# Optimization experiments

Measured on AMD Instinct MI355X. Metric: run time of the kernel, lower is better.

## Reference

```python
import jax, jax.numpy as jnp
import numpy as np

EPS = 1e-5
K = 20
NH = 16
SLOPE = 0.2

def leaky(x):
    return jnp.where(x >= 0, x, SLOPE * x)

def bn(x, g, b, axes):
    # training-mode batch norm (biased variance), channel axis = 1
    m = x.mean(axes, keepdims=True)
    v = x.var(axes, keepdims=True)
    shp = [1] * x.ndim
    shp[1] = -1
    return (x - m) / jnp.sqrt(v + EPS) * g.reshape(shp) + b.reshape(shp)

def efr(x, idx, w, k):
    # x: [B, C, N]; idx: flat global gather indices [B*N*k]; w: [C_out, 2C+1]
    B, C, N = x.shape
    xt = x.transpose(0, 2, 1).reshape(B * N, C)
    feature = xt[idx].reshape(B, N, k, C)            # gathered neighbors
    xc = xt.reshape(B, N, 1, C)
    fmean = feature.mean(-1, keepdims=True)          # [B,N,k,1]
    f = jnp.concatenate([feature - xc, fmean, jnp.broadcast_to(xc, feature.shape)], axis=3)
    return jnp.einsum('bnkc,oc->bonk', f, w)         # 1x1 conv -> [B,C_out,N,k]


def setup_inputs() -> dict:
    key = jax.random.key(0)
    ks = jax.random.split(key, 24)
    B, N = 8, 4096
    IN_CH, FEAT_CH, OUT_CH = 6, 64, 64
    d = {}
    d['points'] = jax.random.normal(ks[0], (B, IN_CH // 2, N), dtype=jnp.float32)
    d['feat'] = jax.random.normal(ks[1], (B, FEAT_CH // 2, N), dtype=jnp.float32)
    d['idx'] = jax.random.randint(ks[2], (B * N * K,), 0, B * N)
    s = 0.1
    d['w_efr_p'] = jax.random.normal(ks[3], (IN_CH, IN_CH + 1), dtype=jnp.float32) * s
    d['w_efr_f'] = jax.random.normal(ks[4], (FEAT_CH, FEAT_CH + 1), dtype=jnp.float32) * s
    d['w_q'] = jax.random.normal(ks[5], (FEAT_CH, FEAT_CH // 2), dtype=jnp.float32) * s
    d['g_q'] = jnp.ones((FEAT_CH,), jnp.float32)
    d['b_q'] = jnp.zeros((FEAT_CH,), jnp.float32)
    d['w_pos1'] = jax.random.normal(ks[6], (IN_CH, IN_CH // 2), dtype=jnp.float32) * s
    d['g_pos1'] = jnp.ones((IN_CH,), jnp.float32)
    d['b_pos1'] = jnp.zeros((IN_CH,), jnp.float32)
    d['w_pos2'] = jax.random.normal(ks[7], (FEAT_CH, IN_CH), dtype=jnp.float32) * s
    d['w_attn'] = jax.random.normal(ks[8], (NH * IN_CH, FEAT_CH), dtype=jnp.float32) * s
    d['g1'] = jnp.ones((NH,), jnp.float32)
    d['b1'] = jnp.zeros((NH,), jnp.float32)
    d['w_lin'] = jax.random.normal(ks[9], (OUT_CH, NH), dtype=jnp.float32) * s
    d['g_lin'] = jnp.ones((OUT_CH,), jnp.float32)
    d['b_lin'] = jnp.zeros((OUT_CH,), jnp.float32)
    d['w_res'] = jax.random.normal(ks[10], (OUT_CH, FEAT_CH), dtype=jnp.float32) * s
    d['g_res'] = jnp.ones((OUT_CH,), jnp.float32)
    d['b_res'] = jnp.zeros((OUT_CH,), jnp.float32)
    return d


def reference(points, feat, idx, w_efr_p, w_efr_f, w_q, g_q, b_q,
              w_pos1, g_pos1, b_pos1, w_pos2, w_attn, g1, b1,
              w_lin, g_lin, b_lin, w_res, g_res, b_res):
    B, _, N = points.shape
    knn_points = efr(points, idx, w_efr_p, K)   # [B,6,N,K]
    knn_feat = efr(feat, idx, w_efr_f, K)       # [B,64,N,K]
    x_q = leaky(bn(jnp.einsum('bcn,oc->bon', feat, w_q), g_q, b_q, (0, 2)))
    pos = leaky(bn(jnp.einsum('bcn,oc->bon', points, w_pos1), g_pos1, b_pos1, (0, 2)))
    pos = pos[:, :, :, None] - knn_points       # [B,6,N,K]
    pos = jnp.einsum('bcnk,oc->bonk', pos, w_pos2)  # [B,64,N,K]
    attn = x_q[:, :, :, None] - knn_feat + pos
    attn = jax.nn.softmax(attn / float(np.sqrt(knn_feat.shape[1])), axis=-1)
    attn = jnp.einsum('bcnk,oc->bonk', attn, w_attn)  # [B,NH*6,N,K]
    attn5 = attn.transpose(0, 2, 3, 1).reshape(B, N, K, NH, -1)  # [B,N,K,NH,6]
    y = jnp.einsum('bnkhc,bcnk->bhnk', attn5, knn_points)        # [B,NH,N,K]
    y = leaky(bn(y, g1, b1, (0, 2, 3)))
    y = bn(jnp.einsum('bcnk,oc->bonk', y, w_lin), g_lin, b_lin, (0, 2, 3))
    res = bn(jnp.einsum('bcnk,oc->bonk', knn_feat, w_res), g_res, b_res, (0, 2, 3))
    y = leaky(y + res)
    return y.max(axis=-1)                        # [B,64,N]
```

## Files before the change

kernel.cpp:

```cpp
#include <hip/hip_runtime.h>

#define KNN 20
#define NN 4096
#define NPTS 32768
#define PPW 8

using short8 = __attribute__((ext_vector_type(8))) short;
using f32x4v = __attribute__((ext_vector_type(4))) float;

__device__ __forceinline__ float lrelu(float x){ return x >= 0.f ? x : 0.2f*x; }
__device__ __forceinline__ unsigned short f2b(float x){
    union { float f; unsigned u; } v; v.f = x;
    unsigned r = v.u + 0x7FFFu + ((v.u >> 16) & 1u);
    return (unsigned short)(r >> 16);
}
__device__ __forceinline__ float b2f(unsigned h){
    union { unsigned u; float f; } v; v.u = h << 16; return v.f;
}
#define WSYNC() do { asm volatile("s_waitcnt lgkmcnt(0)" ::: "memory"); __builtin_amdgcn_sched_barrier(0); } while(0)

__global__ void kprep(const float* __restrict__ weff, const float* __restrict__ wattn,
                      const float* __restrict__ wres,
                      unsigned short* __restrict__ packW, float* __restrict__ wdiff,
                      float* __restrict__ w32t)
{
    int t = threadIdx.x;
    for (int q = t; q < 1536; q += 256){
        int f = q >> 6, l = q & 63;
        const float* W; int n, rowlen, koff;
        if (f < 4){ W = weff; rowlen = 65; n = f*16 + (l&15); koff = 0; }
        else if (f < 16){ W = wattn; rowlen = 64; int ff = f-4; n = (ff>>1)*16 + (l&15); koff = (ff&1)*32; }
        else { W = wres; rowlen = 64; int ff = f-16; n = (ff>>1)*16 + (l&15); koff = (ff&1)*32; }
        #pragma unroll
        for (int j=0;j<8;j++){
            int k = koff + (j>=4?16:0) + 4*(l>>4) + (j&3);
            packW[(size_t)(f*64+l)*8 + j] = f2b(W[n*rowlen + k]);
        }
    }
    for (int q = t; q < 2048; q += 256){
        int c = q >> 5, j = q & 31;
        wdiff[q] = weff[c*65 + 33 + j] - weff[c*65 + j];
    }
    if (t < 64) w32t[t] = weff[t*65 + 32];
}

__global__ void __launch_bounds__(256) k0_prep(
    const float* __restrict__ pts, const float* __restrict__ feat,
    const float* __restrict__ wq, const float* __restrict__ wpos1,
    const float* __restrict__ wefp, const float* __restrict__ wdiff,
    unsigned short* __restrict__ ft16, float* __restrict__ pt4,
    unsigned short* __restrict__ qp16, float* __restrict__ pp,
    unsigned short* __restrict__ base16, float* __restrict__ bpp,
    float* __restrict__ qsum, float* __restrict__ qsq,
    float* __restrict__ psum, float* __restrict__ psq)
{
    __shared__ float swq[2048];
    __shared__ float swd[2048];
    __shared__ float red[4][64], red2[4][64];
    int tid = threadIdx.x;
    for (int m=tid;m<2048;m+=256){ swq[m]=wq[m]; swd[m]=wdiff[m]; }
    __syncthreads();
    int r = blockIdx.x*256 + tid;
    int b = r >> 12, n = r & 4095;
    float p0 = pts[((size_t)b*3+0)*NN+n];
    float p1 = pts[((size_t)b*3+1)*NN+n];
    float p2 = pts[((size_t)b*3+2)*NN+n];
    float pm = (p0+p1+p2)*(1.f/3.f);
    *(float4*)(pt4 + (size_t)r*4) = make_float4(p0,p1,p2,pm);
    float f[32];
    #pragma unroll
    for (int c=0;c<32;c++) f[c] = feat[((size_t)b*32+c)*NN+n];
    #pragma unroll
    for (int c=0;c<32;c+=2){
        unsigned pk = (unsigned)f2b(f[c]) | ((unsigned)f2b(f[c+1])<<16);
        *(unsigned*)(ft16 + (size_t)r*32 + c) = pk;
    }
    float q[64];
    for (int o=0;o<64;o++){
        float a=0.f;
        #pragma unroll
        for (int c=0;c<32;c++) a += swq[o*32+c]*f[c];
        q[o]=a;
    }
    for (int o=0;o<64;o+=2){
        unsigned pk = (unsigned)f2b(q[o]) | ((unsigned)f2b(q[o+1])<<16);
        *(unsigned*)(qp16 + (size_t)r*64 + o) = pk;
    }
    int lane = tid & 63, wvv = tid>>6;
    for (int o=0;o<64;o++){
        float s=q[o], s2=q[o]*q[o];
        for (int d=1; d<64; d<<=1){ s += __shfl_xor(s,d); s2 += __shfl_xor(s2,d); }
        if (lane==0){ red[wvv][o]=s; red2[wvv][o]=s2; }
    }
    __syncthreads();
    if (tid<64){
        atomicAdd(qsum+tid, red[0][tid]+red[1][tid]+red[2][tid]+red[3][tid]);
        atomicAdd(qsq+tid, red2[0][tid]+red2[1][tid]+red2[2][tid]+red2[3][tid]);
    }
    for (int o=0;o<64;o++){
        float a=0.f;
        #pragma unroll
        for (int c=0;c<32;c++) a += swd[o*32+c]*f[c];
        q[o]=a;
    }
    for (int o=0;o<64;o+=2){
        unsigned pk = (unsigned)f2b(q[o]) | ((unsigned)f2b(q[o+1])<<16);
        *(unsigned*)(base16 + (size_t)r*64 + o) = pk;
    }
    float pr[8];
    #pragma unroll
    for (int o=0;o<6;o++) pr[o] = wpos1[o*3]*p0 + wpos1[o*3+1]*p1 + wpos1[o*3+2]*p2;
    pr[6]=0.f; pr[7]=0.f;
    *(float4*)(pp+(size_t)r*8)   = make_float4(pr[0],pr[1],pr[2],pr[3]);
    *(float4*)(pp+(size_t)r*8+4) = make_float4(pr[4],pr[5],pr[6],pr[7]);
    __syncthreads();
    for (int o=0;o<6;o++){
        float s=pr[o], s2=pr[o]*pr[o];
        for (int d=1;d<64;d<<=1){ s += __shfl_xor(s,d); s2 += __shfl_xor(s2,d); }
        if (lane==0){ red[wvv][o]=s; red2[wvv][o]=s2; }
    }
    __syncthreads();
    if (tid<6){
        atomicAdd(psum+tid, red[0][tid]+red[1][tid]+red[2][tid]+red[3][tid]);
        atomicAdd(psq+tid, red2[0][tid]+red2[1][tid]+red2[2][tid]+red2[3][tid]);
    }
    #pragma unroll
    for (int j=0;j<6;j++)
        bpp[(size_t)r*8+j] = p0*(wefp[j*7+4]-wefp[j*7]) + p1*(wefp[j*7+5]-wefp[j*7+1])
                           + p2*(wefp[j*7+6]-wefp[j*7+2]);
    bpp[(size_t)r*8+6]=0.f; bpp[(size_t)r*8+7]=0.f;
}

__global__ void k1_paramsA(
    const float* __restrict__ qsum, const float* __restrict__ qsq,
    const float* __restrict__ psum, const float* __restrict__ psq,
    const float* __restrict__ gq, const float* __restrict__ bq,
    const float* __restrict__ gp, const float* __restrict__ bp,
    float* __restrict__ bnq_a, float* __restrict__ bnq_c,
    float* __restrict__ bnp_a, float* __restrict__ bnp_c)
{
    int t = threadIdx.x;
    const float inv = 1.f/32768.f;
    if (t < 64){
        float m = qsum[t]*inv; float v = qsq[t]*inv - m*m;
        float a = gq[t]*rsqrtf(v + 1e-5f);
        bnq_a[t] = a; bnq_c[t] = bq[t] - m*a;
    }
    if (t < 6){
        float m = psum[t]*inv; float v = psq[t]*inv - m*m;
        float a = gp[t]*rsqrtf(v + 1e-5f);
        bnp_a[t] = a; bnp_c[t] = bp[t] - m*a;
    }
}

#define ARENA 12032
#define ANB 0
#define ATR 2048
#define KFR 6144
#define A2B 0
#define SFM 10240
#define SSKP 10368
#define SNB4 11392
#define SIDX 11904

__global__ void __launch_bounds__(256, 3) k2_main(
    const unsigned short* __restrict__ ft16, const float* __restrict__ pt4,
    const unsigned short* __restrict__ qp16, const float* __restrict__ pp,
    const unsigned short* __restrict__ base16, const float* __restrict__ bpp,
    const int* __restrict__ idx,
    const float* __restrict__ wefp, const float* __restrict__ wpos2,
    const unsigned short* __restrict__ packW, const float* __restrict__ w32t,
    const float* __restrict__ bnq_a, const float* __restrict__ bnq_c,
    const float* __restrict__ bnp_a, const float* __restrict__ bnp_c,
    unsigned short* __restrict__ yv, unsigned short* __restrict__ rf,
    float* __restrict__ yslot, float* __restrict__ rslot)
{
    __shared__ __align__(16) char smem_[4*ARENA];
    const int tid = threadIdx.x;
    const int l = tid & 63, wv = tid >> 6;
    const int lo = l & 15, g = l >> 4;
    char* S = smem_ + wv*ARENA;

    float w2r[4][6], w32r[4];
    #pragma unroll
    for (int nt=0;nt<4;nt++){
        #pragma unroll
        for (int j=0;j<6;j++) w2r[nt][j] = wpos2[(nt*16+lo)*6+j];
        w32r[nt] = w32t[nt*16+lo];
    }
    float ysum=0.f, ysq=0.f;
    float racc[4]={0.f,0.f,0.f,0.f}, rsqa[4]={0.f,0.f,0.f,0.f};

    for (int pi=0; pi<PPW; pi++){
        const int r = blockIdx.x*(4*PPW) + wv*PPW + pi;
        WSYNC();
        if (l < KNN) *(int*)(S+SIDX+l*4) = idx[(size_t)r*KNN + l];
        WSYNC();
        #pragma unroll
        for (int it=0; it<3; it++){
            int id = it*64 + l;
            int k = id >> 3, q = id & 7;
            bool act = id < 160;
            int kk = act ? k : 0;
            int gI = *(const int*)(S+SIDX+kk*4);
            uint2 v; v.x = 0u; v.y = 0u;
            if (act) v = *(const uint2*)(ft16 + (size_t)gI*32 + q*4);
            float s = b2f(v.x & 0xffffu) + b2f(v.x >> 16) + b2f(v.y & 0xffffu) + b2f(v.y >> 16);
            s += __shfl_xor(s,1); s += __shfl_xor(s,2); s += __shfl_xor(s,4);
            if (act){
                if (q == 0) *(float*)(S+SFM+k*4) = s * (1.f/32.f);
                *(uint2*)(S + ANB + (k>>4)*1024 + ((k&15) + 16*(q&3))*16 + (q>>2)*8) = v;
            }
        }
        if (l < KNN){
            int gI = *(const int*)(S+SIDX+l*4);
            *(float4*)(S+SNB4+l*16) = *(const float4*)(pt4 + (size_t)gI*4);
        }
        WSYNC();
        if (l < KNN){
            float4 nb = *(const float4*)(S+SNB4+l*16);
            #pragma unroll
            for (int j=0;j<6;j++){
                float v = bpp[(size_t)r*8+j] + wefp[j*7]*nb.x + wefp[j*7+1]*nb.y
                        + wefp[j*7+2]*nb.z + wefp[j*7+3]*nb.w;
                *(float*)(S+SSKP + (l*8+j)*4) = v;
            }
        }
        float xqv[4], basev[4];
        #pragma unroll
        for (int nt=0;nt<4;nt++){
            int c = nt*16+lo;
            xqv[nt] = lrelu(bnq_a[c]*b2f(qp16[(size_t)r*64+c]) + bnq_c[c]);
            basev[nt] = b2f(base16[(size_t)r*64+c]);
        }
        float sp[6];
        #pragma unroll
        for (int j=0;j<6;j++) sp[j] = lrelu(bnp_a[j]*pp[(size_t)r*8+j] + bnp_c[j]);
        WSYNC();
        f32x4v C1[2][4];
        #pragma unroll
        for (int mt=0;mt<2;mt++)
            #pragma unroll
            for (int nt=0;nt<4;nt++)
                #pragma unroll
                for (int i=0;i<4;i++) C1[mt][nt][i] = 0.f;
        short8 Af[2];
        #pragma unroll
        for (int mt=0;mt<2;mt++) Af[mt] = *(const short8*)(S + ANB + mt*1024 + l*16);
        #pragma unroll
        for (int nt=0;nt<4;nt++){
            short8 Bf = *(const short8*)(packW + (size_t)(nt*64 + l)*8);
            #pragma unroll
            for (int mt=0;mt<2;mt++)
                C1[mt][nt] = __builtin_amdgcn_mfma_f32_16x16x32_bf16(Af[mt], Bf, C1[mt][nt], 0, 0, 0);
        }
        #pragma unroll
        for (int mt=0;mt<2;mt++){
            #pragma unroll
            for (int i=0;i<4;i++){
                int k = mt*16 + g*4 + i;
                bool valid = (k < KNN);
                int kk = valid ? k : 0;
                float fmk = *(const float*)(S+SFM+kk*4);
                float sk[6];
                #pragma unroll
                for (int j=0;j<6;j++) sk[j] = *(const float*)(S+SSKP+(kk*8+j)*4);
                #pragma unroll
                for (int nt=0;nt<4;nt++){
                    float kf = C1[mt][nt][i] + basev[nt] + w32r[nt]*fmk;
                    if (valid){
                        int fragi = mt*2 + (nt>>1);
                        int slot = (g*4+i) + 16*(lo>>2);
                        int jj = (nt&1)*4 + (lo&3);
                        *(unsigned short*)(S + KFR + fragi*1024 + slot*16 + jj*2) = f2b(kf);
                    }
                    float pos = 0.f;
                    #pragma unroll
                    for (int j=0;j<6;j++) pos += (sp[j]-sk[j])*w2r[nt][j];
                    C1[mt][nt][i] = valid ? (xqv[nt] - kf + pos)*0.125f : -1e30f;
                }
            }
        }
        #pragma unroll
        for (int nt=0;nt<4;nt++){
            float mx = -1e30f;
            #pragma unroll
            for (int mt=0;mt<2;mt++)
                #pragma unroll
                for (int i=0;i<4;i++) mx = fmaxf(mx, C1[mt][nt][i]);
            mx = fmaxf(mx, __shfl_xor(mx,16));
            mx = fmaxf(mx, __shfl_xor(mx,32));
            float sm = 0.f;
            #pragma unroll
            for (int mt=0;mt<2;mt++)
                #pragma unroll
                for (int i=0;i<4;i++){ float e = __expf(C1[mt][nt][i]-mx); C1[mt][nt][i]=e; sm += e; }
            sm += __shfl_xor(sm,16);
            sm += __shfl_xor(sm,32);
            float inv = 1.f/sm;
            #pragma unroll
            for (int mt=0;mt<2;mt++)
                #pragma unroll
                for (int i=0;i<4;i++){
                    int k = mt*16 + g*4 + i;
                    if (k < KNN){
                        int fragi = mt*2 + (nt>>1);
                        int slot = (g*4+i) + 16*(lo>>2);
                        int jj = (nt&1)*4 + (lo&3);
                        *(unsigned short*)(S + ATR + fragi*1024 + slot*16 + jj*2) = f2b(C1[mt][nt][i]*inv);
                    }
                }
        }
        WSYNC();
        short8 Aa[2][2];
        #pragma unroll
        for (int mt=0;mt<2;mt++)
            #pragma unroll
            for (int s=0;s<2;s++) Aa[mt][s] = *(const short8*)(S + ATR + (mt*2+s)*1024 + l*16);
        f32x4v C2[2][6];
        #pragma unroll
        for (int mt=0;mt<2;mt++)
            #pragma unroll
            for (int nt=0;nt<6;nt++)
                #pragma unroll
                for (int i=0;i<4;i++) C2[mt][nt][i] = 0.f;
        #pragma unroll
        for (int nt=0;nt<6;nt++){
            #pragma unroll
            for (int s=0;s<2;s++){
                short8 Bf = *(const short8*)(packW + (size_t)((4+nt*2+s)*64 + l)*8);
                #pragma unroll
                for (int mt=0;mt<2;mt++)
                    C2[mt][nt] = __builtin_amdgcn_mfma_f32_16x16x32_bf16(Aa[mt][s], Bf, C2[mt][nt], 0, 0, 0);
            }
        }
        WSYNC();
        #pragma unroll
        for (int mt=0;mt<2;mt++)
            #pragma unroll
            for (int nt=0;nt<6;nt++)
                #pragma unroll
                for (int i=0;i<4;i++){
                    int k = mt*16 + g*4 + i;
                    if (k < KNN){
                        int o = nt*16 + lo;
                        *(unsigned short*)(S + A2B + k*192 + o*2) = f2b(C2[mt][nt][i]);
                    }
                }
        WSYNC();
        #pragma unroll
        for (int it=0; it<5; it++){
            int kq = it*4 + g;
            const char* row = S + A2B + kq*192 + lo*12;
            unsigned d0 = *(const unsigned*)(row);
            unsigned d1 = *(const unsigned*)(row+4);
            unsigned d2 = *(const unsigned*)(row+8);
            float yval = b2f(d0&0xffffu) * (*(const float*)(S+SSKP+(kq*8+0)*4))
                       + b2f(d0>>16)    * (*(const float*)(S+SSKP+(kq*8+1)*4))
                       + b2f(d1&0xffffu)* (*(const float*)(S+SSKP+(kq*8+2)*4))
                       + b2f(d1>>16)    * (*(const float*)(S+SSKP+(kq*8+3)*4))
                       + b2f(d2&0xffffu)* (*(const float*)(S+SSKP+(kq*8+4)*4))
                       + b2f(d2>>16)    * (*(const float*)(S+SSKP+(kq*8+5)*4));
            yv[(size_t)r*320 + lo*KNN + kq] = f2b(yval);
            ysum += yval; ysq += yval*yval;
        }
        short8 Ak[2][2];
        #pragma unroll
        for (int mt=0;mt<2;mt++)
            #pragma unroll
            for (int s=0;s<2;s++) Ak[mt][s] = *(const short8*)(S + KFR + (mt*2+s)*1024 + l*16);
        f32x4v C3[2][4];
        #pragma unroll
        for (int mt=0;mt<2;mt++)
            #pragma unroll
            for (int nt=0;nt<4;nt++)
                #pragma unroll
                for (int i=0;i<4;i++) C3[mt][nt][i] = 0.f;
        #pragma unroll
        for (int nt=0;nt<4;nt++){
            #pragma unroll
            for (int s=0;s<2;s++){
                short8 Bf = *(const short8*)(packW + (size_t)((16+nt*2+s)*64 + l)*8);
                #pragma unroll
                for (int mt=0;mt<2;mt++)
                    C3[mt][nt] = __builtin_amdgcn_mfma_f32_16x16x32_bf16(Ak[mt][s], Bf, C3[mt][nt], 0, 0, 0);
            }
        }
        #pragma unroll
        for (int mt=0;mt<2;mt++)
            #pragma unroll
            for (int i=0;i<4;i++){
                int k = mt*16 + g*4 + i;
                if (k < KNN){
                    #pragma unroll
                    for (int nt=0;nt<4;nt++){
                        float v = C3[mt][nt][i];
                        rf[(size_t)r*1280 + k*64 + nt*16 + lo] = f2b(v);
                        racc[nt] += v; rsqa[nt] += v*v;
                    }
                }
            }
    }
    ysum += __shfl_xor(ysum,16); ysum += __shfl_xor(ysum,32);
    ysq  += __shfl_xor(ysq,16);  ysq  += __shfl_xor(ysq,32);
    #pragma unroll
    for (int nt=0;nt<4;nt++){
        racc[nt] += __shfl_xor(racc[nt],16); racc[nt] += __shfl_xor(racc[nt],32);
        rsqa[nt] += __shfl_xor(rsqa[nt],16); rsqa[nt] += __shfl_xor(rsqa[nt],32);
    }
    int slot = (blockIdx.x*4 + wv) & 63;
    if (l < 16){
        atomicAdd(yslot + slot*32 + l, ysum);
        #pragma unroll
        for (int nt=0;nt<4;nt++) atomicAdd(rslot + slot*128 + nt*16 + l, racc[nt]);
    } else if (l < 32){
        atomicAdd(yslot + slot*32 + 16 + lo, ysq);
        #pragma unroll
        for (int nt=0;nt<4;nt++) atomicAdd(rslot + slot*128 + 64 + nt*16 + lo, rsqa[nt]);
    }
}

__global__ void k3_paramsB(
    const float* __restrict__ yslot, const float* __restrict__ rslot,
    const float* __restrict__ g1, const float* __restrict__ b1,
    const float* __restrict__ gr, const float* __restrict__ br,
    float* __restrict__ bn1_a, float* __restrict__ bn1_c,
    float* __restrict__ bnr_a, float* __restrict__ bnr_c)
{
    __shared__ float sy[32];
    __shared__ float sr[128];
    int t = threadIdx.x;
    float s1 = 0.f;
    if (t < 32){ for (int i=0;i<64;i++) s1 += yslot[(size_t)i*32+t]; }
    float s2 = 0.f;
    for (int i=0;i<64;i++) s2 += rslot[(size_t)i*128+t];
    if (t < 32) sy[t] = s1;
    sr[t] = s2;
    __syncthreads();
    const float inv = 1.f/655360.f;
    if (t < 16){
        float m = sy[t]*inv; float v = sy[16+t]*inv - m*m;
        float a = g1[t]*rsqrtf(v + 1e-5f);
        bn1_a[t] = a; bn1_c[t] = b1[t] - m*a;
    }
    if (t < 64){
        float m = sr[t]*inv; float v = sr[64+t]*inv - m*m;
        float a = gr[t]*rsqrtf(v + 1e-5f);
        bnr_a[t] = a; bnr_c[t] = br[t] - m*a;
    }
}

__global__ void __launch_bounds__(64) k4_linstats(
    const unsigned short* __restrict__ yv,
    const float* __restrict__ bn1_a, const float* __restrict__ bn1_c,
    const float* __restrict__ wl, float* __restrict__ lslot)
{
    __shared__ float sy2[16*KNN];
    const int c = threadIdx.x;
    float wlr[16];
    #pragma unroll
    for (int h=0;h<16;h++) wlr[h] = wl[c*16+h];
    float lsum=0.f, lsq=0.f;
    for (int i=0;i<16;i++){
        size_t r = (size_t)blockIdx.x*16 + i;
        __syncthreads();
        for (int m=c; m<320; m+=64){
            float yy = b2f(yv[r*320+m]);
            int h = m/KNN;
            sy2[m] = lrelu(bn1_a[h]*yy + bn1_c[h]);
        }
        __syncthreads();
        for (int k=0;k<KNN;k++){
            float lv = 0.f;
            #pragma unroll
            for (int h=0;h<16;h++) lv += wlr[h]*sy2[h*KNN+k];
            lsum += lv; lsq += lv*lv;
        }
    }
    atomicAdd(lslot + (size_t)(blockIdx.x&255)*128 + c, lsum);
    atomicAdd(lslot + (size_t)(blockIdx.x&255)*128 + 64 + c, lsq);
}

__global__ void k5_paramsC(
    const float* __restrict__ lslot,
    const float* __restrict__ gl, const float* __restrict__ bl,
    float* __restrict__ bnl_a, float* __restrict__ bnl_c)
{
    __shared__ float sr[128];
    int t = threadIdx.x;
    float s = 0.f;
    for (int i=0;i<256;i++) s += lslot[(size_t)i*128+t];
    sr[t] = s;
    __syncthreads();
    const float inv = 1.f/655360.f;
    if (t < 64){
        float m = sr[t]*inv; float v = sr[64+t]*inv - m*m;
        float a = gl[t]*rsqrtf(v + 1e-5f);
        bnl_a[t] = a; bnl_c[t] = bl[t] - m*a;
    }
}

__global__ void __launch_bounds__(256) k6_final(
    const unsigned short* __restrict__ yv, const unsigned short* __restrict__ rf,
    const float* __restrict__ bn1_a, const float* __restrict__ bn1_c,
    const float* __restrict__ wl,
    const float* __restrict__ bnl_a, const float* __restrict__ bnl_c,
    const float* __restrict__ bnr_a, const float* __restrict__ bnr_c,
    float* __restrict__ out)
{
    __shared__ float sy2[4][16*KNN];
    __shared__ float sout[64][17];
    const int tid = threadIdx.x;
    const int w = tid >> 6, o = tid & 63;
    float wlr[16];
    #pragma unroll
    for (int h=0;h<16;h++) wlr[h] = wl[o*16+h];
    const float la = bnl_a[o], lc = bnl_c[o];
    const float ra = bnr_a[o], rc = bnr_c[o];
    const int r0 = blockIdx.x*16;
    for (int i=0;i<4;i++){
        const size_t r = (size_t)r0 + w*4 + i;
        __syncthreads();
        for (int m=o;m<320;m+=64){
            float yy = b2f(yv[r*320+m]);
            int h = m/KNN;
            sy2[w][m] = lrelu(bn1_a[h]*yy + bn1_c[h]);
        }
        __syncthreads();
        float best = -1e30f;
        for (int k=0;k<KNN;k++){
            float rv = b2f(rf[r*1280 + k*64 + o]);
            float lv = 0.f;
            #pragma unroll
            for (int h=0;h<16;h++) lv += wlr[h]*sy2[w][h*KNN+k];
            float val = lrelu(la*lv + lc + ra*rv + rc);
            best = fmaxf(best, val);
        }
        sout[o][w*4+i] = best;
    }
    __syncthreads();
    const int b = r0 >> 12, n0 = r0 & 4095;
    for (int m=tid;m<1024;m+=256){
        int oo = m >> 4, ii = m & 15;
        out[((size_t)b*64+oo)*NN + n0 + ii] = sout[oo][ii];
    }
}

extern "C" void kernel_launch(void* const* d_in, const int* in_sizes, int n_in,
                              void* d_out, int out_size, void* d_ws, size_t ws_size,
                              hipStream_t stream)
{
    const float* pts   = (const float*)d_in[0];
    const float* feat  = (const float*)d_in[1];
    const int*   idx   = (const int*)d_in[2];
    const float* wefp  = (const float*)d_in[3];
    const float* weff  = (const float*)d_in[4];
    const float* wq    = (const float*)d_in[5];
    const float* gq    = (const float*)d_in[6];
    const float* bq    = (const float*)d_in[7];
    const float* wpos1 = (const float*)d_in[8];
    const float* gp    = (const float*)d_in[9];
    const float* bp    = (const float*)d_in[10];
    const float* wpos2 = (const float*)d_in[11];
    const float* wattn = (const float*)d_in[12];
    const float* g1    = (const float*)d_in[13];
    const float* b1    = (const float*)d_in[14];
    const float* wl    = (const float*)d_in[15];
    const float* gl    = (const float*)d_in[16];
    const float* bl    = (const float*)d_in[17];
    const float* wres  = (const float*)d_in[18];
    const float* gr    = (const float*)d_in[19];
    const float* br    = (const float*)d_in[20];
    float* out = (float*)d_out;

    char* ws = (char*)d_ws;
    size_t o_ft16 = 0;
    size_t o_pt4  = o_ft16 + (size_t)NPTS*32*2;
    size_t o_qp16 = o_pt4  + (size_t)NPTS*4*4;
    size_t o_pp   = o_qp16 + (size_t)NPTS*64*2;
    size_t o_b16  = o_pp   + (size_t)NPTS*8*4;
    size_t o_bpp  = o_b16  + (size_t)NPTS*64*2;
    size_t o_packW= o_bpp  + (size_t)NPTS*8*4;
    size_t o_wdiff= o_packW + 24*512*2;
    size_t o_w32  = o_wdiff + 2048*4;
    size_t o_st   = o_w32   + 64*4;
    size_t o_qsum  = o_st;
    size_t o_qsq   = o_qsum + 64*4;
    size_t o_psum  = o_qsq  + 64*4;
    size_t o_psq   = o_psum + 8*4;
    size_t o_yslot = o_psq  + 8*4;
    size_t o_rslot = o_yslot + (size_t)64*32*4;
    size_t o_lslot = o_rslot + (size_t)64*128*4;
    size_t zero_bytes = (o_lslot + (size_t)256*128*4) - o_st;
    size_t o_par   = o_st + zero_bytes;
    size_t o_bnq_a = o_par;
    size_t o_bnq_c = o_bnq_a + 64*4;
    size_t o_bnp_a = o_bnq_c + 64*4;
    size_t o_bnp_c = o_bnp_a + 8*4;
    size_t o_bn1_a = o_bnp_c + 8*4;
    size_t o_bn1_c = o_bn1_a + 16*4;
    size_t o_bnl_a = o_bn1_c + 16*4;
    size_t o_bnl_c = o_bnl_a + 64*4;
    size_t o_bnr_a = o_bnl_c + 64*4;
    size_t o_bnr_c = o_bnr_a + 64*4;
    size_t o_yv = (o_bnr_c + 64*4 + 255) & ~(size_t)255;
    size_t o_rf = o_yv + (size_t)NPTS*320*2;

    unsigned short* ft16 = (unsigned short*)(ws + o_ft16);
    float* pt4  = (float*)(ws + o_pt4);
    unsigned short* qp16 = (unsigned short*)(ws + o_qp16);
    float* ppb  = (float*)(ws + o_pp);
    unsigned short* b16p = (unsigned short*)(ws + o_b16);
    float* bpp  = (float*)(ws + o_bpp);
    unsigned short* packW = (unsigned short*)(ws + o_packW);
    float* wdiff= (float*)(ws + o_wdiff);
    float* w32t = (float*)(ws + o_w32);
    float* qsum = (float*)(ws + o_qsum);
    float* qsq  = (float*)(ws + o_qsq);
    float* psum = (float*)(ws + o_psum);
    float* psq  = (float*)(ws + o_psq);
    float* yslot= (float*)(ws + o_yslot);
    float* rslot= (float*)(ws + o_rslot);
    float* lslot= (float*)(ws + o_lslot);
    float* bnq_a= (float*)(ws + o_bnq_a);
    float* bnq_c= (float*)(ws + o_bnq_c);
    float* bnp_a= (float*)(ws + o_bnp_a);
    float* bnp_c= (float*)(ws + o_bnp_c);
    float* bn1_a= (float*)(ws + o_bn1_a);
    float* bn1_c= (float*)(ws + o_bn1_c);
    float* bnl_a= (float*)(ws + o_bnl_a);
    float* bnl_c= (float*)(ws + o_bnl_c);
    float* bnr_a= (float*)(ws + o_bnr_a);
    float* bnr_c= (float*)(ws + o_bnr_c);
    unsigned short* yvp = (unsigned short*)(ws + o_yv);
    unsigned short* rfp = (unsigned short*)(ws + o_rf);

    hipMemsetAsync(ws + o_st, 0, zero_bytes, stream);

    kprep<<<1, 256, 0, stream>>>(weff, wattn, wres, packW, wdiff, w32t);
    k0_prep<<<128, 256, 0, stream>>>(pts, feat, wq, wpos1, wefp, wdiff,
                                     ft16, pt4, qp16, ppb, b16p, bpp,
                                     qsum, qsq, psum, psq);
    k1_paramsA<<<1, 64, 0, stream>>>(qsum, qsq, psum, psq, gq, bq, gp, bp,
                                     bnq_a, bnq_c, bnp_a, bnp_c);
    k2_main<<<NPTS/(4*PPW), 256, 0, stream>>>(ft16, pt4, qp16, ppb, b16p, bpp, idx,
                                     wefp, wpos2, packW, w32t,
                                     bnq_a, bnq_c, bnp_a, bnp_c,
                                     yvp, rfp, yslot, rslot);
    k3_paramsB<<<1, 128, 0, stream>>>(yslot, rslot, g1, b1, gr, br,
                                      bn1_a, bn1_c, bnr_a, bnr_c);
    k4_linstats<<<2048, 64, 0, stream>>>(yvp, bn1_a, bn1_c, wl, lslot);
    k5_paramsC<<<1, 128, 0, stream>>>(lslot, gl, bl, bnl_a, bnl_c);
    k6_final<<<2048, 256, 0, stream>>>(yvp, rfp, bn1_a, bn1_c, wl,
                                       bnl_a, bnl_c, bnr_a, bnr_c, out);
}
```

Baseline: 537.4 us.

## Prefetch next-point gathers, swizzle LDS fragments, stage outputs, compute linear BN stats via Gram matrix

The main kernel now preloads all gather indices once and issues the global gathers for the next point before computing the current one, so load latency overlaps with MFMA work. Fragment layouts in LDS are XOR-swizzled to reduce bank conflicts. The y and residual outputs are staged in LDS and written with vectorized nontemporal stores, and y is now stored point-major by k. Linear-layer batch-norm statistics are computed from a 16x16 Gram matrix and channel sums accumulated with MFMA, then projected through the weights in the params kernel. This adds register pressure and restructures several kernels together.

```diff
diff --git a/kernel.cpp b/kernel.cpp
--- a/kernel.cpp
+++ b/kernel.cpp
@@ -7,6 +7,7 @@
 
 using short8 = __attribute__((ext_vector_type(8))) short;
 using f32x4v = __attribute__((ext_vector_type(4))) float;
+using uint4v = __attribute__((ext_vector_type(4))) unsigned int;
 
 __device__ __forceinline__ float lrelu(float x){ return x >= 0.f ? x : 0.2f*x; }
 __device__ __forceinline__ unsigned short f2b(float x){
@@ -18,6 +19,10 @@
     union { unsigned u; float f; } v; v.u = h << 16; return v.f;
 }
 #define WSYNC() do { asm volatile("s_waitcnt lgkmcnt(0)" ::: "memory"); __builtin_amdgcn_sched_barrier(0); } while(0)
+
+__device__ __forceinline__ int fslot(int fragi, int klocal, int gp){
+    return fragi*1024 + (((klocal) + ((gp)<<4)) ^ ((gp)*5))*16;
+}
 
 __global__ void kprep(const float* __restrict__ weff, const float* __restrict__ wattn,
                       const float* __restrict__ wres,
@@ -153,15 +158,14 @@
     }
 }
 
-#define ARENA 12032
-#define ANB 0
-#define ATR 2048
-#define KFR 6144
-#define A2B 0
-#define SFM 10240
-#define SSKP 10368
-#define SNB4 11392
-#define SIDX 11904
+#define ARENA 12544
+#define ANB   0
+#define ATR   2048
+#define KFR   6272
+#define SFM   10368
+#define SSKP  10496
+#define SIDX  11136
+#define YST   11776
 
 __global__ void __launch_bounds__(256, 3) k2_main(
     const unsigned short* __restrict__ ft16, const float* __restrict__ pt4,
@@ -180,63 +184,87 @@
     const int l = tid & 63, wv = tid >> 6;
     const int lo = l & 15, g = l >> 4;
     char* S = smem_ + wv*ARENA;
-
-    float w2r[4][6], w32r[4];
+    const int srd = (l ^ (g*5))*16;
+
+    float w2r[4][6], w32r[4], bnqa[4], bnqc[4];
     #pragma unroll
     for (int nt=0;nt<4;nt++){
         #pragma unroll
         for (int j=0;j<6;j++) w2r[nt][j] = wpos2[(nt*16+lo)*6+j];
         w32r[nt] = w32t[nt*16+lo];
-    }
+        bnqa[nt] = bnq_a[nt*16+lo];
+        bnqc[nt] = bnq_c[nt*16+lo];
+    }
+    float bnpa[6], bnpc[6];
+    #pragma unroll
+    for (int j=0;j<6;j++){ bnpa[j]=bnp_a[j]; bnpc[j]=bnp_c[j]; }
+
     float ysum=0.f, ysq=0.f;
     float racc[4]={0.f,0.f,0.f,0.f}, rsqa[4]={0.f,0.f,0.f,0.f};
 
+    const int rbase = blockIdx.x*(4*PPW) + wv*PPW;
+
+    *(int*)(S+SIDX+l*4)        = idx[(size_t)rbase*KNN + l];
+    *(int*)(S+SIDX+(64+l)*4)   = idx[(size_t)rbase*KNN + 64 + l];
+    if (l < 32) *(int*)(S+SIDX+(128+l)*4) = idx[(size_t)rbase*KNN + 128 + l];
+    WSYNC();
+
+    uint2 ng0, ng1; uint2 ng2 = make_uint2(0u,0u); float4 ngp4 = make_float4(0,0,0,0);
+    unsigned short nqr[4], nbr[4];
+    float nppr[6], nbppr[6];
+    float xqv[4], basev[4], sp[6];
+
+#define ISSUE(pi_) { \
+    int sb = (pi_)*KNN*4; size_t rr = (size_t)(rbase + (pi_)); \
+    int i0 = *(const int*)(S+SIDX+sb+(l>>3)*4); \
+    int i1 = *(const int*)(S+SIDX+sb+(8+(l>>3))*4); \
+    ng0 = *(const uint2*)(ft16 + (size_t)i0*32 + (l&7)*4); \
+    ng1 = *(const uint2*)(ft16 + (size_t)i1*32 + (l&7)*4); \
+    if (l < 32){ int i2 = *(const int*)(S+SIDX+sb+(16+(l>>3))*4); \
+                 ng2 = *(const uint2*)(ft16 + (size_t)i2*32 + (l&7)*4); } \
+    if (l < KNN){ int ip = *(const int*)(S+SIDX+sb+l*4); \
+                  ngp4 = *(const float4*)(pt4 + (size_t)ip*4); } \
+    _Pragma("unroll") for (int nt=0;nt<4;nt++){ \
+        nqr[nt] = qp16[rr*64 + nt*16+lo]; nbr[nt] = base16[rr*64 + nt*16+lo]; } \
+    _Pragma("unroll") for (int j=0;j<6;j++){ nppr[j] = pp[rr*8+j]; nbppr[j] = bpp[rr*8+j]; } \
+    __builtin_amdgcn_sched_barrier(0); \
+}
+
+#define STAGE() { \
+    float s0 = b2f(ng0.x&0xffffu)+b2f(ng0.x>>16)+b2f(ng0.y&0xffffu)+b2f(ng0.y>>16); \
+    float s1 = b2f(ng1.x&0xffffu)+b2f(ng1.x>>16)+b2f(ng1.y&0xffffu)+b2f(ng1.y>>16); \
+    float s2 = b2f(ng2.x&0xffffu)+b2f(ng2.x>>16)+b2f(ng2.y&0xffffu)+b2f(ng2.y>>16); \
+    s0 += __shfl_xor(s0,1); s0 += __shfl_xor(s0,2); s0 += __shfl_xor(s0,4); \
+    s1 += __shfl_xor(s1,1); s1 += __shfl_xor(s1,2); s1 += __shfl_xor(s1,4); \
+    s2 += __shfl_xor(s2,1); s2 += __shfl_xor(s2,2); s2 += __shfl_xor(s2,4); \
+    if ((l&7)==0){ \
+        *(float*)(S+SFM+(l>>3)*4) = s0*(1.f/32.f); \
+        *(float*)(S+SFM+(8+(l>>3))*4) = s1*(1.f/32.f); \
+        if (l < 32) *(float*)(S+SFM+(16+(l>>3))*4) = s2*(1.f/32.f); \
+    } \
+    { int kk = l>>3, gp_ = l&3, jb = ((l>>2)&1)*8; \
+      *(uint2*)(S + ANB + fslot(0, kk, gp_) + jb) = ng0; \
+      *(uint2*)(S + ANB + fslot(0, 8+kk, gp_) + jb) = ng1; \
+      if (l < 32) *(uint2*)(S + ANB + fslot(1, kk, gp_) + jb) = ng2; } \
+    if (l < KNN){ \
+        _Pragma("unroll") for (int j=0;j<6;j++){ \
+            float v = nbppr[j] + wefp[j*7]*ngp4.x + wefp[j*7+1]*ngp4.y \
+                    + wefp[j*7+2]*ngp4.z + wefp[j*7+3]*ngp4.w; \
+            *(float*)(S+SSKP+(l*8+j)*4) = v; } } \
+    _Pragma("unroll") for (int nt=0;nt<4;nt++){ \
+        xqv[nt] = lrelu(bnqa[nt]*b2f(nqr[nt]) + bnqc[nt]); \
+        basev[nt] = b2f(nbr[nt]); } \
+    _Pragma("unroll") for (int j=0;j<6;j++) sp[j] = lrelu(bnpa[j]*nppr[j] + bnpc[j]); \
+    WSYNC(); \
+}
+
+    ISSUE(0);
+    STAGE();
+
     for (int pi=0; pi<PPW; pi++){
-        const int r = blockIdx.x*(4*PPW) + wv*PPW + pi;
-        WSYNC();
-        if (l < KNN) *(int*)(S+SIDX+l*4) = idx[(size_t)r*KNN + l];
-        WSYNC();
-        #pragma unroll
-        for (int it=0; it<3; it++){
-            int id = it*64 + l;
-            int k = id >> 3, q = id & 7;
-            bool act = id < 160;
-            int kk = act ? k : 0;
-            int gI = *(const int*)(S+SIDX+kk*4);
-            uint2 v; v.x = 0u; v.y = 0u;
-            if (act) v = *(const uint2*)(ft16 + (size_t)gI*32 + q*4);
-            float s = b2f(v.x & 0xffffu) + b2f(v.x >> 16) + b2f(v.y & 0xffffu) + b2f(v.y >> 16);
-            s += __shfl_xor(s,1); s += __shfl_xor(s,2); s += __shfl_xor(s,4);
-            if (act){
-                if (q == 0) *(float*)(S+SFM+k*4) = s * (1.f/32.f);
-                *(uint2*)(S + ANB + (k>>4)*1024 + ((k&15) + 16*(q&3))*16 + (q>>2)*8) = v;
-            }
-        }
-        if (l < KNN){
-            int gI = *(const int*)(S+SIDX+l*4);
-            *(float4*)(S+SNB4+l*16) = *(const float4*)(pt4 + (size_t)gI*4);
-        }
-        WSYNC();
-        if (l < KNN){
-            float4 nb = *(const float4*)(S+SNB4+l*16);
-            #pragma unroll
-            for (int j=0;j<6;j++){
-                float v = bpp[(size_t)r*8+j] + wefp[j*7]*nb.x + wefp[j*7+1]*nb.y
-                        + wefp[j*7+2]*nb.z + wefp[j*7+3]*nb.w;
-                *(float*)(S+SSKP + (l*8+j)*4) = v;
-            }
-        }
-        float xqv[4], basev[4];
-        #pragma unroll
-        for (int nt=0;nt<4;nt++){
-            int c = nt*16+lo;
-            xqv[nt] = lrelu(bnq_a[c]*b2f(qp16[(size_t)r*64+c]) + bnq_c[c]);
-            basev[nt] = b2f(base16[(size_t)r*64+c]);
-        }
-        float sp[6];
-        #pragma unroll
-        for (int j=0;j<6;j++) sp[j] = lrelu(bnp_a[j]*pp[(size_t)r*8+j] + bnp_c[j]);
-        WSYNC();
+        const size_t r = (size_t)(rbase + pi);
+        if (pi < PPW-1) ISSUE(pi+1);
+
         f32x4v C1[2][4];
         #pragma unroll
         for (int mt=0;mt<2;mt++)
@@ -244,15 +272,13 @@
             for (int nt=0;nt<4;nt++)
                 #pragma unroll
                 for (int i=0;i<4;i++) C1[mt][nt][i] = 0.f;
-        short8 Af[2];
-        #pragma unroll
-        for (int mt=0;mt<2;mt++) Af[mt] = *(const short8*)(S + ANB + mt*1024 + l*16);
+        short8 Af0 = *(const short8*)(S + ANB + 0*1024 + srd);
+        short8 Af1 = *(const short8*)(S + ANB + 1*1024 + srd);
         #pragma unroll
         for (int nt=0;nt<4;nt++){
             short8 Bf = *(const short8*)(packW + (size_t)(nt*64 + l)*8);
-            #pragma unroll
-            for (int mt=0;mt<2;mt++)
-                C1[mt][nt] = __builtin_amdgcn_mfma_f32_16x16x32_bf16(Af[mt], Bf, C1[mt][nt], 0, 0, 0);
+            C1[0][nt] = __builtin_amdgcn_mfma_f32_16x16x32_bf16(Af0, Bf, C1[0][nt], 0, 0, 0);
+            C1[1][nt] = __builtin_amdgcn_mfma_f32_16x16x32_bf16(Af1, Bf, C1[1][nt], 0, 0, 0);
         }
         #pragma unroll
         for (int mt=0;mt<2;mt++){
@@ -269,10 +295,8 @@
                 for (int nt=0;nt<4;nt++){
                     float kf = C1[mt][nt][i] + basev[nt] + w32r[nt]*fmk;
                     if (valid){
-                        int fragi = mt*2 + (nt>>1);
-                        int slot = (g*4+i) + 16*(lo>>2);
-                        int jj = (nt&1)*4 + (lo&3);
-                        *(unsigned short*)(S + KFR + fragi*1024 + slot*16 + jj*2) = f2b(kf);
+                        int fa = fslot(mt*2+(nt>>1), g*4+i, lo>>2) + ((nt&1)*4 + (lo&3))*2;
+                        *(unsigned short*)(S + KFR + fa) = f2b(kf);
                     }
                     float pos = 0.f;
                     #pragma unroll
@@ -304,10 +328,8 @@
                 for (int i=0;i<4;i++){
                     int k = mt*16 + g*4 + i;
                     if (k < KNN){
-                        int fragi = mt*2 + (nt>>1);
-                        int slot = (g*4+i) + 16*(lo>>2);
-                        int jj = (nt&1)*4 + (lo&3);
-                        *(unsigned short*)(S + ATR + fragi*1024 + slot*16 + jj*2) = f2b(C1[mt][nt][i]*inv);
+                        int fa = fslot(mt*2+(nt>>1), g*4+i, lo>>2) + ((nt&1)*4 + (lo&3))*2;
+                        *(unsigned short*)(S + ATR + fa) = f2b(C1[mt][nt][i]*inv);
                     }
                 }
         }
@@ -316,7 +338,7 @@
         #pragma unroll
         for (int mt=0;mt<2;mt++)
             #pragma unroll
-            for (int s=0;s<2;s++) Aa[mt][s] = *(const short8*)(S + ATR + (mt*2+s)*1024 + l*16);
+            for (int s=0;s<2;s++) Aa[mt][s] = *(const short8*)(S + ATR + (mt*2+s)*1024 + srd);
         f32x4v C2[2][6];
         #pragma unroll
         for (int mt=0;mt<2;mt++)
@@ -342,16 +364,14 @@
                 #pragma unroll
                 for (int i=0;i<4;i++){
                     int k = mt*16 + g*4 + i;
-                    if (k < KNN){
-                        int o = nt*16 + lo;
-                        *(unsigned short*)(S + A2B + k*192 + o*2) = f2b(C2[mt][nt][i]);
-                    }
+                    if (k < KNN)
+                        *(unsigned short*)(S + ATR + k*208 + (nt*16+lo)*2) = f2b(C2[mt][nt][i]);
                 }
         WSYNC();
         #pragma unroll
         for (int it=0; it<5; it++){
             int kq = it*4 + g;
-            const char* row = S + A2B + kq*192 + lo*12;
+            const char* row = S + ATR + kq*208 + lo*12;
             unsigned d0 = *(const unsigned*)(row);
             unsigned d1 = *(const unsigned*)(row+4);
             unsigned d2 = *(const unsigned*)(row+8);
@@ -361,14 +381,14 @@
                        + b2f(d1>>16)    * (*(const float*)(S+SSKP+(kq*8+3)*4))
                        + b2f(d2&0xffffu)* (*(const float*)(S+SSKP+(kq*8+4)*4))
                        + b2f(d2>>16)    * (*(const float*)(S+SSKP+(kq*8+5)*4));
-            yv[(size_t)r*320 + lo*KNN + kq] = f2b(yval);
+            *(unsigned short*)(S + YST + kq*32 + lo*2) = f2b(yval);
             ysum += yval; ysq += yval*yval;
         }
         short8 Ak[2][2];
         #pragma unroll
         for (int mt=0;mt<2;mt++)
             #pragma unroll
-            for (int s=0;s<2;s++) Ak[mt][s] = *(const short8*)(S + KFR + (mt*2+s)*1024 + l*16);
+            for (int s=0;s<2;s++) Ak[mt][s] = *(const short8*)(S + KFR + (mt*2+s)*1024 + srd);
         f32x4v C3[2][4];
         #pragma unroll
         for (int mt=0;mt<2;mt++)
@@ -386,6 +406,7 @@
                     C3[mt][nt] = __builtin_amdgcn_mfma_f32_16x16x32_bf16(Ak[mt][s], Bf, C3[mt][nt], 0, 0, 0);
             }
         }
+        WSYNC();
         #pragma unroll
         for (int mt=0;mt<2;mt++)
             #pragma unroll
@@ -395,11 +416,26 @@
                     #pragma unroll
                     for (int nt=0;nt<4;nt++){
                         float v = C3[mt][nt][i];
-                        rf[(size_t)r*1280 + k*64 + nt*16 + lo] = f2b(v);
+                        *(unsigned short*)(S + ATR + k*144 + (nt*16+lo)*2) = f2b(v);
                         racc[nt] += v; rsqa[nt] += v*v;
                     }
                 }
             }
+        WSYNC();
+        if (l < 40){
+            uint4v v = *(const uint4v*)(S + YST + l*16);
+            __builtin_nontemporal_store(v, (uint4v*)((char*)yv + r*640 + l*16));
+        }
+        #pragma unroll
+        for (int t=0;t<3;t++){
+            int s = t*64 + l;
+            if (s < 160){
+                int kk = s>>3, pt_ = s&7;
+                uint4v v = *(const uint4v*)(S + ATR + kk*144 + pt_*16);
+                __builtin_nontemporal_store(v, (uint4v*)((char*)rf + r*2560 + kk*128 + pt_*16));
+            }
+        }
+        if (pi < PPW-1) STAGE();
     }
     ysum += __shfl_xor(ysum,16); ysum += __shfl_xor(ysum,32);
     ysq  += __shfl_xor(ysq,16);  ysq  += __shfl_xor(ysq,32);
@@ -418,6 +454,8 @@
         #pragma unroll
         for (int nt=0;nt<4;nt++) atomicAdd(rslot + slot*128 + 64 + nt*16 + lo, rsqa[nt]);
     }
+#undef ISSUE
+#undef STAGE
 }
 
 __global__ void k3_paramsB(
@@ -450,53 +488,93 @@
     }
 }
 
-__global__ void __launch_bounds__(64) k4_linstats(
+__global__ void __launch_bounds__(256) k4_linstats(
     const unsigned short* __restrict__ yv,
     const float* __restrict__ bn1_a, const float* __restrict__ bn1_c,
-    const float* __restrict__ wl, float* __restrict__ lslot)
-{
-    __shared__ float sy2[16*KNN];
-    const int c = threadIdx.x;
-    float wlr[16];
-    #pragma unroll
-    for (int h=0;h<16;h++) wlr[h] = wl[c*16+h];
-    float lsum=0.f, lsq=0.f;
-    for (int i=0;i<16;i++){
-        size_t r = (size_t)blockIdx.x*16 + i;
-        __syncthreads();
-        for (int m=c; m<320; m+=64){
-            float yy = b2f(yv[r*320+m]);
-            int h = m/KNN;
-            sy2[m] = lrelu(bn1_a[h]*yy + bn1_c[h]);
-        }
-        __syncthreads();
-        for (int k=0;k<KNN;k++){
-            float lv = 0.f;
-            #pragma unroll
-            for (int h=0;h<16;h++) lv += wlr[h]*sy2[h*KNN+k];
-            lsum += lv; lsq += lv*lv;
-        }
-    }
-    atomicAdd(lslot + (size_t)(blockIdx.x&255)*128 + c, lsum);
-    atomicAdd(lslot + (size_t)(blockIdx.x&255)*128 + 64 + c, lsq);
+    float* __restrict__ Mslot, float* __restrict__ Sslot)
+{
+    __shared__ __align__(16) char lds[4*1024];
+    const int tid = threadIdx.x, l = tid & 63, wvv = tid >> 6;
+    const int lo = l & 15, g = l >> 4;
+    char* L = lds + wvv*1024;
+    const int h0 = (l&1)*8;
+    float a8[8], c8[8];
+    #pragma unroll
+    for (int j=0;j<8;j++){ a8[j]=bn1_a[h0+j]; c8[j]=bn1_c[h0+j]; }
+    short8 ones;
+    #pragma unroll
+    for (int j=0;j<8;j++) ones[j] = (short)0x3F80;
+    f32x4v Macc, Sacc;
+    #pragma unroll
+    for (int i=0;i<4;i++){ Macc[i]=0.f; Sacc[i]=0.f; }
+    const int waveid = blockIdx.x*4 + wvv;
+    for (int it=0; it<5; it++){
+        size_t s0 = ((size_t)waveid*5 + it)*32;
+        uint4 v = *(const uint4*)(yv + s0*16 + l*8);
+        unsigned short e0 = v.x&0xffffu, e1 = v.x>>16, e2 = v.y&0xffffu, e3 = v.y>>16;
+        unsigned short e4 = v.z&0xffffu, e5 = v.z>>16, e6 = v.w&0xffffu, e7 = v.w>>16;
+        float y0 = lrelu(a8[0]*b2f(e0)+c8[0]), y1 = lrelu(a8[1]*b2f(e1)+c8[1]);
+        float y2_ = lrelu(a8[2]*b2f(e2)+c8[2]), y3 = lrelu(a8[3]*b2f(e3)+c8[3]);
+        float y4 = lrelu(a8[4]*b2f(e4)+c8[4]), y5 = lrelu(a8[5]*b2f(e5)+c8[5]);
+        float y6 = lrelu(a8[6]*b2f(e6)+c8[6]), y7 = lrelu(a8[7]*b2f(e7)+c8[7]);
+        uint4 o;
+        o.x = (unsigned)f2b(y0) | ((unsigned)f2b(y1)<<16);
+        o.y = (unsigned)f2b(y2_)| ((unsigned)f2b(y3)<<16);
+        o.z = (unsigned)f2b(y4) | ((unsigned)f2b(y5)<<16);
+        o.w = (unsigned)f2b(y6) | ((unsigned)f2b(y7)<<16);
+        *(uint4*)(L + l*16) = o;
+        WSYNC();
+        short8 Af;
+        #pragma unroll
+        for (int j=0;j<8;j++){
+            int s = 4*g + (j&3) + ((j>=4)?16:0);
+            Af[j] = *(const short*)(L + s*32 + lo*2);
+        }
+        WSYNC();
+        Macc = __builtin_amdgcn_mfma_f32_16x16x32_bf16(Af, Af, Macc, 0, 0, 0);
+        Sacc = __builtin_amdgcn_mfma_f32_16x16x32_bf16(ones, Af, Sacc, 0, 0, 0);
+    }
+    float* Ms = Mslot + (size_t)(waveid&15)*256;
+    #pragma unroll
+    for (int i=0;i<4;i++) atomicAdd(Ms + (g*4+i)*16 + lo, Macc[i]);
+    if (l < 16) atomicAdd(Sslot + (size_t)(waveid&15)*16 + lo, Sacc[0]);
 }
 
 __global__ void k5_paramsC(
-    const float* __restrict__ lslot,
+    const float* __restrict__ Mslot, const float* __restrict__ Sslot,
+    const float* __restrict__ wl,
     const float* __restrict__ gl, const float* __restrict__ bl,
     float* __restrict__ bnl_a, float* __restrict__ bnl_c)
 {
-    __shared__ float sr[128];
+    __shared__ float Ms[256], Ss[16];
     int t = threadIdx.x;
-    float s = 0.f;
-    for (int i=0;i<256;i++) s += lslot[(size_t)i*128+t];
-    sr[t] = s;
+    float m = 0.f;
+    for (int i=0;i<16;i++) m += Mslot[(size_t)i*256+t];
+    Ms[t] = m;
+    if (t < 16){
+        float s = 0.f;
+        for (int i=0;i<16;i++) s += Sslot[(size_t)i*16+t];
+        Ss[t] = s;
+    }
     __syncthreads();
-    const float inv = 1.f/655360.f;
     if (t < 64){
-        float m = sr[t]*inv; float v = sr[64+t]*inv - m*m;
-        float a = gl[t]*rsqrtf(v + 1e-5f);
-        bnl_a[t] = a; bnl_c[t] = bl[t] - m*a;
+        float w[16];
+        #pragma unroll
+        for (int h=0;h<16;h++) w[h] = wl[t*16+h];
+        float lsum = 0.f;
+        #pragma unroll
+        for (int h=0;h<16;h++) lsum += w[h]*Ss[h];
+        float lsq = 0.f;
+        for (int h1=0;h1<16;h1++){
+            float acc = 0.f;
+            #pragma unroll
+            for (int h2=0;h2<16;h2++) acc += Ms[h1*16+h2]*w[h2];
+            lsq += w[h1]*acc;
+        }
+        const float inv = 1.f/655360.f;
+        float mean = lsum*inv; float var = lsq*inv - mean*mean;
+        float a = gl[t]*rsqrtf(var + 1e-5f);
+        bnl_a[t] = a; bnl_c[t] = bl[t] - mean*a;
     }
 }
 
@@ -523,16 +601,17 @@
         __syncthreads();
         for (int m=o;m<320;m+=64){
             float yy = b2f(yv[r*320+m]);
-            int h = m/KNN;
+            int h = m & 15;
             sy2[w][m] = lrelu(bn1_a[h]*yy + bn1_c[h]);
         }
         __syncthreads();
         float best = -1e30f;
         for (int k=0;k<KNN;k++){
-            float rv = b2f(rf[r*1280 + k*64 + o]);
+            unsigned short rv16 = __builtin_nontemporal_load(rf + r*1280 + k*64 + o);
+            float rv = b2f(rv16);
             float lv = 0.f;
             #pragma unroll
-            for (int h=0;h<16;h++) lv += wlr[h]*sy2[w][h*KNN+k];
+            for (int h=0;h<16;h++) lv += wlr[h]*sy2[w][k*16+h];
             float val = lrelu(la*lv + lc + ra*rv + rc);
             best = fmaxf(best, val);
         }
@@ -590,8 +669,9 @@
     size_t o_psq   = o_psum + 8*4;
     size_t o_yslot = o_psq  + 8*4;
     size_t o_rslot = o_yslot + (size_t)64*32*4;
-    size_t o_lslot = o_rslot + (size_t)64*128*4;
-    size_t zero_bytes = (o_lslot + (size_t)256*128*4) - o_st;
+    size_t o_mslot = o_rslot + (size_t)64*128*4;
+    size_t o_sslot = o_mslot + (size_t)16*256*4;
+    size_t zero_bytes = (o_sslot + (size_t)16*16*4) - o_st;
     size_t o_par   = o_st + zero_bytes;
     size_t o_bnq_a = o_par;
     size_t o_bnq_c = o_bnq_a + 64*4;
@@ -611,7 +691,7 @@
     unsigned short* qp16 = (unsigned short*)(ws + o_qp16);
     float* ppb  = (float*)(ws + o_pp);
     unsigned short* b16p = (unsigned short*)(ws + o_b16);
-    float* bpp  = (float*)(ws + o_bpp);
+    float* bppb = (float*)(ws + o_bpp);
     unsigned short* packW = (unsigned short*)(ws + o_packW);
     float* wdiff= (float*)(ws + o_wdiff);
     float* w32t = (float*)(ws + o_w32);
@@ -621,7 +701,8 @@
     float* psq  = (float*)(ws + o_psq);
     float* yslot= (float*)(ws + o_yslot);
     float* rslot= (float*)(ws + o_rslot);
-    float* lslot= (float*)(ws + o_lslot);
+    float* Mslot= (float*)(ws + o_mslot);
+    float* Sslot= (float*)(ws + o_sslot);
     float* bnq_a= (float*)(ws + o_bnq_a);
     float* bnq_c= (float*)(ws + o_bnq_c);
     float* bnp_a= (float*)(ws + o_bnp_a);
@@ -635,22 +716,22 @@
     unsigned short* yvp = (unsigned short*)(ws + o_yv);
     unsigned short* rfp = (unsigned short*)(ws + o_rf);
 
-    hipMemsetAsync(ws + o_st, 0, zero_bytes, stream);
+    (void)hipMemsetAsync(ws + o_st, 0, zero_bytes, stream);
 
     kprep<<<1, 256, 0, stream>>>(weff, wattn, wres, packW, wdiff, w32t);
     k0_prep<<<128, 256, 0, stream>>>(pts, feat, wq, wpos1, wefp, wdiff,
-                                     ft16, pt4, qp16, ppb, b16p, bpp,
+                                     ft16, pt4, qp16, ppb, b16p, bppb,
                                      qsum, qsq, psum, psq);
     k1_paramsA<<<1, 64, 0, stream>>>(qsum, qsq, psum, psq, gq, bq, gp, bp,
                                      bnq_a, bnq_c, bnp_a, bnp_c);
-    k2_main<<<NPTS/(4*PPW), 256, 0, stream>>>(ft16, pt4, qp16, ppb, b16p, bpp, idx,
+    k2_main<<<NPTS/(4*PPW), 256, 0, stream>>>(ft16, pt4, qp16, ppb, b16p, bppb, idx,
                                      wefp, wpos2, packW, w32t,
                                      bnq_a, bnq_c, bnp_a, bnp_c,
                                      yvp, rfp, yslot, rslot);
     k3_paramsB<<<1, 128, 0, stream>>>(yslot, rslot, g1, b1, gr, br,
                                       bn1_a, bn1_c, bnr_a, bnr_c);
-    k4_linstats<<<2048, 64, 0, stream>>>(yvp, bn1_a, bn1_c, wl, lslot);
-    k5_paramsC<<<1, 128, 0, stream>>>(lslot, gl, bl, bnl_a, bnl_c);
+    k4_linstats<<<1024, 256, 0, stream>>>(yvp, bn1_a, bn1_c, Mslot, Sslot);
+    k5_paramsC<<<1, 256, 0, stream>>>(Mslot, Sslot, wl, gl, bl, bnl_a, bnl_c);
     k6_final<<<2048, 256, 0, stream>>>(yvp, rfp, bn1_a, bn1_c, wl,
                                        bnl_a, bnl_c, bnr_a, bnr_c, out);
 }
```

New measurement: 549.1 us. 2.2% more time.
